# Kernel tuning notes

Measured on AMD Instinct MI355X. Metric: run time of the kernel, lower is better.

Reference implementation:

```python
import jax, jax.numpy as jnp
import numpy as np

B, N, DIM, H, DH = 8, 1024, 1024, 16, 64

def setup_inputs() -> dict:
    key = jax.random.key(0)
    ks = jax.random.split(key, 6)
    return {
        'x': jax.random.normal(ks[0], (B, N, DIM), dtype=jnp.float32),
        'freqs': jax.random.normal(ks[1], (1, N, DH), dtype=jnp.float32),
        'bias': jax.random.normal(ks[2], (1, N, DH), dtype=jnp.float32),
        'ln_gamma': jnp.ones((DIM,), jnp.float32),
        'ln_beta': jnp.zeros((DIM,), jnp.float32),
        'w_qk': jax.random.normal(ks[3], (DIM, 2 * H * DH), dtype=jnp.float32) * (DIM ** -0.5),
        'w_v': jax.random.normal(ks[4], (DIM, H * DH), dtype=jnp.float32) * (DIM ** -0.5),
        'w_out': jax.random.normal(ks[5], (H * DH, DIM), dtype=jnp.float32) * ((H * DH) ** -0.5),
        'b_out': jnp.zeros((DIM,), jnp.float32),
    }

def _apply_polar(t, freqs):
    # t: [b,h,n,d]; freqs: [1,n,d] broadcast over b,h. Output doubles last dim.
    t = jax.nn.softplus(t)
    return jnp.concatenate((t * jnp.cos(freqs), t * jnp.sin(freqs)), axis=-1)

def reference(x, freqs, bias, ln_gamma, ln_beta, w_qk, w_v, w_out, b_out):
    eps = 1e-5
    mu = jnp.mean(x, axis=-1, keepdims=True)
    var = jnp.var(x, axis=-1, keepdims=True)
    xn = (x - mu) * jax.lax.rsqrt(var + eps) * ln_gamma + ln_beta
    qk = jnp.einsum('bnd,de->bne', xn, w_qk)
    q, k = jnp.split(qk, 2, axis=-1)
    v = jnp.einsum('bnd,de->bne', xn, w_v)
    split_heads = lambda t: t.reshape(B, N, H, DH).transpose(0, 2, 1, 3)
    q, k, v = split_heads(q), split_heads(k), split_heads(v)
    q = _apply_polar(q, freqs)          # [b,h,n,2*DH]
    k = _apply_polar(k, freqs + bias)   # [b,h,n,2*DH]
    scale = DH ** -0.5
    dots = jnp.einsum('bhnd,bhmd->bhnm', q, k) * scale
    attn = jax.nn.softmax(dots, axis=-1)
    out = jnp.einsum('bhnm,bhmd->bhnd', attn, v)
    out = out.transpose(0, 2, 1, 3).reshape(B, N, H * DH)
    return jnp.einsum('bne,ed->bnd', out, w_out) + b_out
```

## Files before the change

kernel.cpp:

```cpp
#include <hip/hip_runtime.h>
#include <cmath>

using f16   = _Float16;
using f16x2 = __attribute__((ext_vector_type(2))) _Float16;
using f16x4 = __attribute__((ext_vector_type(4))) _Float16;
using f16x8 = __attribute__((ext_vector_type(8))) _Float16;
using f32x4 = __attribute__((ext_vector_type(4))) float;

#define DEV __device__ __forceinline__

constexpr int Bb  = 8;
constexpr int Nn  = 1024;
constexpr int DIM = 1024;
constexpr int Hh  = 16;
constexpr int DH  = 64;
constexpr int EQKV = 3072;

DEV void async16(const f16* g, f16* l) {
  __builtin_amdgcn_global_load_lds(
      (const __attribute__((address_space(1))) void*)g,
      (__attribute__((address_space(3))) void*)l, 16, 0, 0);
}

DEV float softplusf(float x) {
  return fmaxf(x, 0.f) + __logf(1.f + __expf(-fabsf(x)));
}

__global__ __launch_bounds__(256) void transpose_cvt3(const float* __restrict__ s0,
                                                      const float* __restrict__ s1,
                                                      const float* __restrict__ s2,
                                                      f16* __restrict__ d0,
                                                      f16* __restrict__ d2) {
  __shared__ float tile[32][33];
  const float* src; f16* dst; int cols;
  int bz = blockIdx.z;
  if (bz == 0)      { src = s0; dst = d0;                        cols = 2048; }
  else if (bz == 1) { src = s1; dst = d0 + (size_t)2048 * 1024;  cols = 1024; }
  else              { src = s2; dst = d2;                        cols = 1024; }
  int c0 = blockIdx.x * 32, r0 = blockIdx.y * 32;
  if (c0 >= cols) return;
  int t = threadIdx.x, tx = t & 31, ty = t >> 5;
#pragma unroll
  for (int j = 0; j < 32; j += 8)
    tile[ty + j][tx] = src[(size_t)(r0 + ty + j) * cols + c0 + tx];
  __syncthreads();
#pragma unroll
  for (int j = 0; j < 32; j += 8)
    dst[(size_t)(c0 + ty + j) * 1024 + r0 + tx] = (f16)tile[tx][ty + j];
}

__global__ __launch_bounds__(256) void ln_kernel(const float* __restrict__ x,
                                                 const float* __restrict__ gamma,
                                                 const float* __restrict__ beta,
                                                 f16* __restrict__ xn) {
  int row = blockIdx.x;
  int t = threadIdx.x;
  const float4* xr = (const float4*)(x + (size_t)row * DIM);
  float4 v = xr[t];
  float s  = v.x + v.y + v.z + v.w;
  float s2 = v.x * v.x + v.y * v.y + v.z * v.z + v.w * v.w;
#pragma unroll
  for (int off = 32; off; off >>= 1) {
    s  += __shfl_xor(s,  off, 64);
    s2 += __shfl_xor(s2, off, 64);
  }
  __shared__ float red[8];
  int wv = t >> 6, lane = t & 63;
  if (lane == 0) { red[wv] = s; red[4 + wv] = s2; }
  __syncthreads();
  s  = red[0] + red[1] + red[2] + red[3];
  s2 = red[4] + red[5] + red[6] + red[7];
  float mu  = s * (1.f / DIM);
  float var = s2 * (1.f / DIM) - mu * mu;
  float rs  = rsqrtf(var + 1e-5f);
  float4 g = ((const float4*)gamma)[t];
  float4 bb = ((const float4*)beta)[t];
  f16x4 o;
  o[0] = (f16)((v.x - mu) * rs * g.x + bb.x);
  o[1] = (f16)((v.y - mu) * rs * g.y + bb.y);
  o[2] = (f16)((v.z - mu) * rs * g.z + bb.z);
  o[3] = (f16)((v.w - mu) * rs * g.w + bb.w);
  ((f16x4*)(xn + (size_t)row * DIM))[t] = o;
}

template <bool FP32OUT>
__global__ __launch_bounds__(256) void gemm_bt(const f16* __restrict__ A,
                                               const f16* __restrict__ Bt,
                                               void* __restrict__ Cv,
                                               const float* __restrict__ bias,
                                               int M, int K, int E) {
  __shared__ f16 lA[128 * 32];
  __shared__ f16 lB[128 * 32];
  int tid  = threadIdx.x;
  int lane = tid & 63;
  int wv   = __builtin_amdgcn_readfirstlane(tid >> 6);
  int nbe  = E >> 7;
  int bm = blockIdx.x / nbe, be = blockIdx.x % nbe;
  size_t m0 = (size_t)bm * 128, e0 = (size_t)be * 128;
  int wm = (wv & 1) * 64, we = (wv >> 1) * 64;
  int lm = lane & 15, q = lane >> 4;

  f32x4 acc[4][4] = {};

  int row_s[2], cg_s[2];
#pragma unroll
  for (int r = 0; r < 2; ++r) {
    int s = r * 256 + tid;
    row_s[r] = s >> 2;
    cg_s[r]  = (s & 3) ^ ((row_s[r] >> 1) & 3);
  }
  const f16* pa[4];
  const f16* pb[4];
#pragma unroll
  for (int i = 0; i < 4; ++i) {
    int ra = wm + i * 16 + lm;
    pa[i] = lA + ra * 32 + (q ^ ((ra >> 1) & 3)) * 8;
    int rb = we + i * 16 + lm;
    pb[i] = lB + rb * 32 + (q ^ ((rb >> 1) & 3)) * 8;
  }

  for (int k0 = 0; k0 < K; k0 += 32) {
#pragma unroll
    for (int r = 0; r < 2; ++r) {
      const f16* ga = A  + (m0 + row_s[r]) * K + k0 + cg_s[r] * 8;
      const f16* gb = Bt + (e0 + row_s[r]) * K + k0 + cg_s[r] * 8;
      async16(ga, lA + (r * 256 + wv * 64) * 8);
      async16(gb, lB + (r * 256 + wv * 64) * 8);
    }
    __syncthreads();
    f16x8 af[4], bf[4];
#pragma unroll
    for (int i = 0; i < 4; ++i) {
      af[i] = *(const f16x8*)pa[i];
      bf[i] = *(const f16x8*)pb[i];
    }
#pragma unroll
    for (int i = 0; i < 4; ++i)
#pragma unroll
      for (int j = 0; j < 4; ++j)
        acc[i][j] = __builtin_amdgcn_mfma_f32_16x16x32_f16(af[i], bf[j], acc[i][j], 0, 0, 0);
    __syncthreads();
  }

#pragma unroll
  for (int i = 0; i < 4; ++i) {
    size_t mbase = m0 + wm + i * 16 + q * 4;
#pragma unroll
    for (int j = 0; j < 4; ++j) {
      size_t e = e0 + we + j * 16 + lm;
#pragma unroll
      for (int g = 0; g < 4; ++g) {
        float val = acc[i][j][g];
        if (FP32OUT)
          ((float*)Cv)[(mbase + g) * (size_t)E + e] = val + bias[e];
        else
          ((f16*)Cv)[(mbase + g) * (size_t)E + e] = (f16)val;
      }
    }
  }
}

__global__ __launch_bounds__(256) void polar_kernel(const f16* __restrict__ qkv,
                                                    const float* __restrict__ freqs,
                                                    const float* __restrict__ fbias,
                                                    f16* __restrict__ Qp,
                                                    f16* __restrict__ Kp,
                                                    f16* __restrict__ Vt) {
  __shared__ f16 vt[64 * 66];
  int tid = threadIdx.x;
  int bx = blockIdx.x;
  int nt = bx & 15, bh = bx >> 4;
  int b = bh >> 4, h = bh & 15;
  size_t tok0 = (size_t)b * Nn + nt * 64;
  int n0 = nt * 64;
  constexpr float kScale = 0.125f;
#pragma unroll
  for (int i = 0; i < 8; ++i) {
    int e2 = tid + i * 256;
    int nl = e2 >> 5, dp = (e2 & 31) * 2;
    size_t src = (tok0 + nl) * EQKV + h * 64 + dp;
    f16x2 q2 = *(const f16x2*)(qkv + src);
    f16x2 k2 = *(const f16x2*)(qkv + src + 1024);
    f16x2 v2 = *(const f16x2*)(qkv + src + 2048);
    int fidx = (n0 + nl) * 64 + dp;
    float2 f2  = *(const float2*)(freqs + fidx);
    float2 fb2 = *(const float2*)(fbias + fidx);
    f16x2 qc, qs, kc, ksn;
#pragma unroll
    for (int u = 0; u < 2; ++u) {
      float fq = u ? f2.y : f2.x;
      float fk = fq + (u ? fb2.y : fb2.x);
      float spq = softplusf((float)q2[u]) * kScale;
      float spk = softplusf((float)k2[u]);
      float snq, csq, snk, csk;
      __sincosf(fq, &snq, &csq);
      __sincosf(fk, &snk, &csk);
      qc[u]  = (f16)(spq * csq);
      qs[u]  = (f16)(spq * snq);
      kc[u]  = (f16)(spk * csk);
      ksn[u] = (f16)(spk * snk);
    }
    size_t dst = ((size_t)bh * Nn + n0 + nl) * 128 + dp;
    *(f16x2*)(Qp + dst)      = qc;
    *(f16x2*)(Qp + dst + 64) = qs;
    *(f16x2*)(Kp + dst)      = kc;
    *(f16x2*)(Kp + dst + 64) = ksn;
    vt[dp * 66 + nl]       = v2[0];
    vt[(dp + 1) * 66 + nl] = v2[1];
  }
  __syncthreads();
#pragma unroll
  for (int i = 0; i < 16; ++i) {
    int e = tid + i * 256;
    int d = e >> 6, nl = e & 63;
    Vt[((size_t)bh * 64 + d) * Nn + n0 + nl] = vt[d * 66 + nl];
  }
}

constexpr int VK0 = 0;
constexpr int VK1 = 8192;
constexpr int VV0 = 16384;
constexpr int VV1 = 21504;
constexpr int VEND = 26624;

__global__ __launch_bounds__(256, 3) void attn_kernel(const f16* __restrict__ Qp,
                                                      const f16* __restrict__ Kp,
                                                      const f16* __restrict__ Vt,
                                                      f16* __restrict__ attout) {
  __shared__ f16 smem[VEND];

  int tid = threadIdx.x, lane = tid & 63;
  int wv = __builtin_amdgcn_readfirstlane(tid >> 6);
  int lm = lane & 15, q = lane >> 4;
  int bx = blockIdx.x;
  int bh = (bx & 7) | ((bx >> 6) << 3);
  int qt = (bx >> 3) & 7;
  const f16* Kbase = Kp + (size_t)bh * Nn * 128;
  const f16* Vbase = Vt + (size_t)bh * 64 * Nn;

  {
    int idx = tid * 4;
    f16 val = (idx < 64) ? (f16)1.0f : (f16)0.0f;
    f16x4 v4 = {val, val, val, val};
    *(f16x4*)(smem + VV0 + 64 * 64 + idx) = v4;
    *(f16x4*)(smem + VV1 + 64 * 64 + idx) = v4;
  }

#pragma unroll
  for (int i = 0; i < 4; ++i) {
    int s = i * 256 + tid;
    int r = s >> 4, c = s & 15;
    int g = c ^ (r & 15);
    async16(Kbase + (size_t)r * 128 + g * 8, smem + VK0 + (i * 256 + wv * 64) * 8);
  }
#pragma unroll
  for (int i = 0; i < 2; ++i) {
    int s = i * 256 + tid;
    int r = s >> 3, c = s & 7;
    int g = c ^ (r & 7);
    async16(Vbase + (size_t)r * Nn + g * 8, smem + VV0 + (i * 256 + wv * 64) * 8);
  }

  f16x8 qf[2][4];
  {
    const f16* Qb = Qp + ((size_t)bh * Nn + qt * 128 + wv * 32) * 128;
#pragma unroll
    for (int grp = 0; grp < 2; ++grp)
#pragma unroll
      for (int ks = 0; ks < 4; ++ks)
        qf[grp][ks] = *(const f16x8*)(Qb + (size_t)(grp * 16 + lm) * 128 + ks * 32 + q * 8);
  }

  f32x4 O[2][5] = {};
  float mrow[2] = {-INFINITY, -INFINITY};

  for (int kt = 0; kt < 16; ++kt) {
    __syncthreads();

    if (kt < 15) {
      f16* nK = smem + ((kt & 1) ? VK0 : VK1);
      f16* nV = smem + ((kt & 1) ? VV0 : VV1);
#pragma unroll
      for (int i = 0; i < 4; ++i) {
        int s = i * 256 + tid;
        int r = s >> 4, c = s & 15;
        int g = c ^ (r & 15);
        async16(Kbase + (size_t)((kt + 1) * 64 + r) * 128 + g * 8, nK + (i * 256 + wv * 64) * 8);
      }
#pragma unroll
      for (int i = 0; i < 2; ++i) {
        int s = i * 256 + tid;
        int r = s >> 3, c = s & 7;
        int g = c ^ (r & 7);
        async16(Vbase + (size_t)r * Nn + (kt + 1) * 64 + g * 8, nV + (i * 256 + wv * 64) * 8);
      }
    }
    const f16* sK = smem + ((kt & 1) ? VK1 : VK0);
    const f16* sV = smem + ((kt & 1) ? VV1 : VV0);

    f32x4 S[2][4] = {};
#pragma unroll
    for (int nt = 0; nt < 4; ++nt) {
      f16x8 kf[4];
#pragma unroll
      for (int ks = 0; ks < 4; ++ks)
        kf[ks] = *(const f16x8*)(sK + (nt * 16 + lm) * 128 + (((ks * 4 + q) ^ lm) * 8));
#pragma unroll
      for (int ks = 0; ks < 4; ++ks) {
        S[0][nt] = __builtin_amdgcn_mfma_f32_16x16x32_f16(kf[ks], qf[0][ks], S[0][nt], 0, 0, 0);
        S[1][nt] = __builtin_amdgcn_mfma_f32_16x16x32_f16(kf[ks], qf[1][ks], S[1][nt], 0, 0, 0);
      }
    }

    f16x4 pf[2][4];
#pragma unroll
    for (int grp = 0; grp < 2; ++grp) {
      float mx = -INFINITY;
#pragma unroll
      for (int nt = 0; nt < 4; ++nt)
#pragma unroll
        for (int g = 0; g < 4; ++g) mx = fmaxf(mx, S[grp][nt][g]);
      mx = fmaxf(mx, __shfl_xor(mx, 16, 64));
      mx = fmaxf(mx, __shfl_xor(mx, 32, 64));
      float mn = fmaxf(mrow[grp], mx);
      float alpha = __expf(mrow[grp] - mn);
      mrow[grp] = mn;
#pragma unroll
      for (int nt = 0; nt < 4; ++nt)
#pragma unroll
        for (int g = 0; g < 4; ++g)
          pf[grp][nt][g] = (f16)__expf(S[grp][nt][g] - mn);
#pragma unroll
      for (int nto = 0; nto < 5; ++nto)
#pragma unroll
        for (int g = 0; g < 4; ++g) O[grp][nto][g] *= alpha;
    }

#pragma unroll
    for (int nto = 0; nto < 5; ++nto) {
      int r = nto * 16 + lm;
#pragma unroll
      for (int nt = 0; nt < 4; ++nt) {
        int c16 = (nt * 2 + (q >> 1)) ^ (r & 7);
        f16x4 vf = *(const f16x4*)(sV + r * 64 + c16 * 8 + (q & 1) * 4);
        O[0][nto] = __builtin_amdgcn_mfma_f32_16x16x16f16(vf, pf[0][nt], O[0][nto], 0, 0, 0);
        O[1][nto] = __builtin_amdgcn_mfma_f32_16x16x16f16(vf, pf[1][nt], O[1][nto], 0, 0, 0);
      }
    }
  }

  int b = bh >> 4, h = bh & 15;
#pragma unroll
  for (int grp = 0; grp < 2; ++grp) {
    float l = __shfl(O[grp][4][0], lm, 64);
    float inv = 1.f / l;
    size_t token = (size_t)b * Nn + qt * 128 + wv * 32 + grp * 16 + lm;
#pragma unroll
    for (int nto = 0; nto < 4; ++nto) {
      f16x4 o4;
#pragma unroll
      for (int g = 0; g < 4; ++g) o4[g] = (f16)(O[grp][nto][g] * inv);
      *(f16x4*)(attout + token * (size_t)(Hh * DH) + h * 64 + nto * 16 + q * 4) = o4;
    }
  }
}

extern "C" void kernel_launch(void* const* d_in, const int* in_sizes, int n_in,
                              void* d_out, int out_size, void* d_ws, size_t ws_size,
                              hipStream_t stream) {
  const float* x     = (const float*)d_in[0];
  const float* freqs = (const float*)d_in[1];
  const float* fbias = (const float*)d_in[2];
  const float* gamma = (const float*)d_in[3];
  const float* beta  = (const float*)d_in[4];
  const float* w_qk  = (const float*)d_in[5];
  const float* w_v   = (const float*)d_in[6];
  const float* w_out = (const float*)d_in[7];
  const float* b_out = (const float*)d_in[8];
  float* out = (float*)d_out;

  const size_t T = (size_t)Bb * Nn;
  f16* WqkvT = (f16*)d_ws;
  f16* WoutT = WqkvT + (size_t)EQKV * DIM;
  f16* Xn    = WoutT + (size_t)DIM * DIM;
  f16* QKV   = Xn + T * DIM;
  f16* AttO  = QKV + T * EQKV;
  f16* Qp    = AttO + T * DIM;
  f16* Kp    = Qp + (size_t)128 * Nn * 128;
  f16* Vt    = Kp + (size_t)128 * Nn * 128;

  transpose_cvt3<<<dim3(64, 32, 3), 256, 0, stream>>>(w_qk, w_v, w_out, WqkvT, WoutT);

  ln_kernel<<<(int)T, 256, 0, stream>>>(x, gamma, beta, Xn);

  gemm_bt<false><<<(int)(T / 128) * (EQKV / 128), 256, 0, stream>>>(
      Xn, WqkvT, (void*)QKV, nullptr, (int)T, DIM, EQKV);

  polar_kernel<<<Bb * Hh * (Nn / 64), 256, 0, stream>>>(QKV, freqs, fbias, Qp, Kp, Vt);

  attn_kernel<<<Bb * Hh * (Nn / 128), 256, 0, stream>>>(Qp, Kp, Vt, AttO);

  gemm_bt<true><<<(int)(T / 128) * (DIM / 128), 256, 0, stream>>>(
      AttO, WoutT, (void*)out, b_out, (int)T, DIM, DIM);
}
```

Baseline: 312.8 us.

## Use 256x256-tile double-buffered GEMM with staged async loads for QKV projection

Adds a new 512-thread GEMM kernel with 256x256 output tiles, an XOR-swizzled LDS layout, double buffering, and global_load_lds prefetches split into stages that interleave with MFMA groups. A block-id swizzle groups tiles for L2 locality. It replaces the 128x128 GEMM for the QKV projection only, aiming for higher arithmetic intensity and better overlap of loads with compute. The cost is 128KB of LDS per block and a larger accumulator register footprint, which may limit occupancy.

Result: faster. 301.5 us (-3.6%).

```diff
diff --git a/kernel.cpp b/kernel.cpp
--- a/kernel.cpp
+++ b/kernel.cpp
@@ -160,6 +160,150 @@
   }
 }
 
+template <bool FP32OUT>
+__global__ __launch_bounds__(512, 2) void gemm256(const f16* __restrict__ A,
+                                                  const f16* __restrict__ Bt,
+                                                  void* __restrict__ Cv,
+                                                  const float* __restrict__ bias,
+                                                  int M, int K, int E) {
+  __shared__ f16 sm[65536];
+  const int tid  = threadIdx.x;
+  const int lane = tid & 63;
+  const int wv   = __builtin_amdgcn_readfirstlane(tid >> 6);
+  const int lm   = lane & 15, q = lane >> 4;
+  const int wrow = (wv >> 2) * 128;
+  const int wcol = (wv & 3) * 64;
+
+  const int nbe = E >> 8;
+  const int cpx = gridDim.x >> 3;
+  const int bid = blockIdx.x;
+  const int swz = (bid & 7) * cpx + (bid >> 3);
+  const int bm = swz / nbe, be = swz % nbe;
+  const size_t m0 = (size_t)bm * 256, e0 = (size_t)be * 256;
+
+  const int rl  = lane >> 3;
+  const int pcp = lane & 7;
+  const int cg  = pcp ^ rl;
+  const f16* aS = A  + (m0 + (size_t)(wv * 8 + rl)) * K + cg * 8;
+  const f16* bS = Bt + (e0 + (size_t)((wv >> 2) * 64 + (wv & 3) * 8 + rl)) * K + cg * 8;
+  const int aDofs = wv * 512;
+  const int bDofs = 16384 + ((wv >> 2) * 64 + (wv & 3) * 8) * 64;
+
+  const int x0 = ((0 + q) ^ (lm & 7)) * 8;
+  const int x1 = ((4 + q) ^ (lm & 7)) * 8;
+
+  const int NT = K >> 6;
+
+  async16(aS,                     sm + aDofs);
+  async16(aS + (size_t)128 * K,   sm + aDofs + 128 * 64);
+  async16(bS,                     sm + bDofs);
+  async16(bS + (size_t)128 * K,   sm + bDofs + 128 * 64);
+  async16(bS + (size_t)32 * K,    sm + bDofs + 32 * 64);
+  async16(bS + (size_t)160 * K,   sm + bDofs + 160 * 64);
+  async16(aS + (size_t)64 * K,    sm + aDofs + 64 * 64);
+  async16(aS + (size_t)192 * K,   sm + aDofs + 192 * 64);
+
+  f32x4 acc[8][4] = {};
+  f16x8 af[4][2], bf[4][2];
+
+  for (int t = 0; t < NT; ++t) {
+    const int b = t & 1, nb = b ^ 1;
+    const int tn = (t + 1 < NT) ? t + 1 : t;
+    const f16* pA = sm + b * 32768;
+    const f16* pB = pA + 16384;
+    f16* aD = sm + nb * 32768 + aDofs;
+    f16* bD = sm + nb * 32768 + bDofs;
+    const f16* aSk = aS + tn * 64;
+    const f16* bSk = bS + tn * 64;
+
+    async16(aSk,                   aD);
+    async16(aSk + (size_t)128 * K, aD + 128 * 64);
+    asm volatile("s_waitcnt vmcnt(6)" ::: "memory");
+    __builtin_amdgcn_s_barrier();
+#pragma unroll
+    for (int i = 0; i < 4; ++i) {
+      const f16* p = pA + (wrow + i * 16 + lm) * 64;
+      af[i][0] = *(const f16x8*)(p + x0);
+      af[i][1] = *(const f16x8*)(p + x1);
+    }
+#pragma unroll
+    for (int j = 0; j < 2; ++j) {
+      const f16* p = pB + (wcol + j * 16 + lm) * 64;
+      bf[j][0] = *(const f16x8*)(p + x0);
+      bf[j][1] = *(const f16x8*)(p + x1);
+    }
+    __builtin_amdgcn_s_setprio(1);
+#pragma unroll
+    for (int i = 0; i < 4; ++i)
+#pragma unroll
+      for (int j = 0; j < 2; ++j) {
+        acc[i][j] = __builtin_amdgcn_mfma_f32_16x16x32_f16(af[i][0], bf[j][0], acc[i][j], 0, 0, 0);
+        acc[i][j] = __builtin_amdgcn_mfma_f32_16x16x32_f16(af[i][1], bf[j][1], acc[i][j], 0, 0, 0);
+      }
+    __builtin_amdgcn_s_setprio(0);
+
+    async16(bSk,                   bD);
+    async16(bSk + (size_t)128 * K, bD + 128 * 64);
+    asm volatile("s_waitcnt vmcnt(6)" ::: "memory");
+    __builtin_amdgcn_s_barrier();
+#pragma unroll
+    for (int j = 0; j < 2; ++j) {
+      const f16* p = pB + (wcol + 32 + j * 16 + lm) * 64;
+      bf[2 + j][0] = *(const f16x8*)(p + x0);
+      bf[2 + j][1] = *(const f16x8*)(p + x1);
+    }
+    __builtin_amdgcn_s_setprio(1);
+#pragma unroll
+    for (int i = 0; i < 4; ++i)
+#pragma unroll
+      for (int j = 2; j < 4; ++j) {
+        acc[i][j] = __builtin_amdgcn_mfma_f32_16x16x32_f16(af[i][0], bf[j][0], acc[i][j], 0, 0, 0);
+        acc[i][j] = __builtin_amdgcn_mfma_f32_16x16x32_f16(af[i][1], bf[j][1], acc[i][j], 0, 0, 0);
+      }
+    __builtin_amdgcn_s_setprio(0);
+
+    async16(bSk + (size_t)32 * K,  bD + 32 * 64);
+    async16(bSk + (size_t)160 * K, bD + 160 * 64);
+    async16(aSk + (size_t)64 * K,  aD + 64 * 64);
+    async16(aSk + (size_t)192 * K, aD + 192 * 64);
+    asm volatile("s_waitcnt vmcnt(8)" ::: "memory");
+    __builtin_amdgcn_s_barrier();
+#pragma unroll
+    for (int i = 0; i < 4; ++i) {
+      const f16* p = pA + (wrow + 64 + i * 16 + lm) * 64;
+      af[i][0] = *(const f16x8*)(p + x0);
+      af[i][1] = *(const f16x8*)(p + x1);
+    }
+    __builtin_amdgcn_s_setprio(1);
+#pragma unroll
+    for (int i = 0; i < 4; ++i)
+#pragma unroll
+      for (int j = 0; j < 4; ++j) {
+        acc[4 + i][j] = __builtin_amdgcn_mfma_f32_16x16x32_f16(af[i][0], bf[j][0], acc[4 + i][j], 0, 0, 0);
+        acc[4 + i][j] = __builtin_amdgcn_mfma_f32_16x16x32_f16(af[i][1], bf[j][1], acc[4 + i][j], 0, 0, 0);
+      }
+    __builtin_amdgcn_s_setprio(0);
+  }
+  asm volatile("s_waitcnt vmcnt(0)" ::: "memory");
+
+#pragma unroll
+  for (int ii = 0; ii < 8; ++ii) {
+    size_t mrow = m0 + wrow + (ii >> 2) * 64 + (ii & 3) * 16 + q * 4;
+#pragma unroll
+    for (int j = 0; j < 4; ++j) {
+      size_t e = e0 + wcol + j * 16 + lm;
+#pragma unroll
+      for (int g = 0; g < 4; ++g) {
+        float val = acc[ii][j][g];
+        if (FP32OUT)
+          ((float*)Cv)[(mrow + g) * (size_t)E + e] = val + bias[e];
+        else
+          ((f16*)Cv)[(mrow + g) * (size_t)E + e] = (f16)val;
+      }
+    }
+  }
+}
+
 __global__ __launch_bounds__(256) void polar_kernel(const f16* __restrict__ qkv,
                                                     const float* __restrict__ freqs,
                                                     const float* __restrict__ fbias,
@@ -393,7 +537,7 @@
 
   ln_kernel<<<(int)T, 256, 0, stream>>>(x, gamma, beta, Xn);
 
-  gemm_bt<false><<<(int)(T / 128) * (EQKV / 128), 256, 0, stream>>>(
+  gemm256<false><<<(int)(T / 256) * (EQKV / 256), 512, 0, stream>>>(
       Xn, WqkvT, (void*)QKV, nullptr, (int)T, DIM, EQKV);
 
   polar_kernel<<<Bb * Hh * (Nn / 64), 256, 0, stream>>>(QKV, freqs, fbias, Qp, Kp, Vt);
```

## Fuse softplus-polar epilogue into a wider-tile QKV GEMM with a precomputed trig table

Applied to the files above, without the earlier changes.

Replaces the generic QKV GEMM plus the separate polar kernel with a dedicated 128x256-tile GEMM. Its epilogue applies softplus, the q scale and cos/sin directly, writing Qp/Kp in an interleaved (cos,sin) layout. V is written in plain token-major form and transposed by a slimmed kernel. A small prep kernel precomputes cos/sin of freqs and freqs+bias once into a float4 table. The goal is to avoid writing and re-reading the full fp16 QKV intermediate and to recompute no trig per batch/head. The cost is a heavier epilogue with scattered 4-byte stores, extra registers from the larger tile, and one extra tiny launch.

Result: slower. 394.5 us (+26.1%).

```diff
diff --git a/kernel.cpp b/kernel.cpp
--- a/kernel.cpp
+++ b/kernel.cpp
@@ -47,6 +47,17 @@
 #pragma unroll
   for (int j = 0; j < 32; j += 8)
     dst[(size_t)(c0 + ty + j) * 1024 + r0 + tx] = (f16)tile[tx][ty + j];
+}
+
+__global__ __launch_bounds__(256) void trig_prep(const float* __restrict__ freqs,
+                                                 const float* __restrict__ fbias,
+                                                 float4* __restrict__ trig) {
+  int i = blockIdx.x * 256 + threadIdx.x;
+  float f = freqs[i], fb = fbias[i];
+  float cq, sq, ck, sk;
+  __sincosf(f, &sq, &cq);
+  __sincosf(f + fb, &sk, &ck);
+  trig[i] = make_float4(cq, sq, ck, sk);
 }
 
 __global__ __launch_bounds__(256) void ln_kernel(const float* __restrict__ x,
@@ -160,12 +171,121 @@
   }
 }
 
-__global__ __launch_bounds__(256) void polar_kernel(const f16* __restrict__ qkv,
-                                                    const float* __restrict__ freqs,
-                                                    const float* __restrict__ fbias,
-                                                    f16* __restrict__ Qp,
-                                                    f16* __restrict__ Kp,
-                                                    f16* __restrict__ Vt) {
+__global__ __launch_bounds__(256, 3) void gemm_qkv(const f16* __restrict__ A,
+                                                   const f16* __restrict__ Bt,
+                                                   f16* __restrict__ Qp,
+                                                   f16* __restrict__ Kp,
+                                                   f16* __restrict__ Vn,
+                                                   const float4* __restrict__ trig,
+                                                   int M, int K) {
+  __shared__ f16 sm[24576];
+  const int tid  = threadIdx.x;
+  const int lane = tid & 63;
+  const int wv   = __builtin_amdgcn_readfirstlane(tid >> 6);
+  const int lm   = lane & 15, q = lane >> 4;
+  const int wrow = (wv >> 1) * 64;
+  const int wcol = (wv & 1) * 128;
+
+  const int nbe = EQKV >> 8;
+  const int cpx = gridDim.x >> 3;
+  const int bid = blockIdx.x;
+  const int swz = (bid & 7) * cpx + (bid >> 3);
+  const int bm = swz / nbe, be = swz % nbe;
+  const size_t m0 = (size_t)bm * 128, e0 = (size_t)be * 256;
+
+  const int rl = tid >> 2, pc = tid & 3;
+  const int cg = pc ^ ((rl >> 1) & 3);
+  const f16* aS = A  + (m0 + rl) * K + cg * 8;
+  const f16* bS = Bt + (e0 + rl) * K + cg * 8;
+  const int aDo = tid * 8;
+  const int bDo = 4096 + tid * 8;
+
+  const int x = (q ^ ((lm >> 1) & 3)) * 8;
+
+  const int NT = K >> 5;
+
+  async16(aS,                  sm + aDo);
+  async16(aS + (size_t)64 * K, sm + aDo + 2048);
+  async16(bS,                  sm + bDo);
+  async16(bS + (size_t)64 * K, sm + bDo + 2048);
+  async16(bS + (size_t)128 * K, sm + bDo + 4096);
+  async16(bS + (size_t)192 * K, sm + bDo + 6144);
+
+  f32x4 acc[4][8] = {};
+
+  for (int t = 0; t < NT; ++t) {
+    const int b = t & 1;
+    __syncthreads();
+
+    if (t + 1 < NT) {
+      f16* nB = sm + (b ^ 1) * 12288;
+      const int k = (t + 1) * 32;
+      async16(aS + k,                  nB + aDo);
+      async16(aS + (size_t)64 * K + k, nB + aDo + 2048);
+      async16(bS + k,                  nB + bDo);
+      async16(bS + (size_t)64 * K + k, nB + bDo + 2048);
+      async16(bS + (size_t)128 * K + k, nB + bDo + 4096);
+      async16(bS + (size_t)192 * K + k, nB + bDo + 6144);
+    }
+
+    const f16* pA = sm + b * 12288;
+    const f16* pB = pA + 4096;
+    f16x8 bf[8], af[4];
+#pragma unroll
+    for (int j = 0; j < 8; ++j)
+      bf[j] = *(const f16x8*)(pB + (wcol + j * 16 + lm) * 32 + x);
+#pragma unroll
+    for (int i = 0; i < 4; ++i)
+      af[i] = *(const f16x8*)(pA + (wrow + i * 16 + lm) * 32 + x);
+#pragma unroll
+    for (int i = 0; i < 4; ++i)
+#pragma unroll
+      for (int j = 0; j < 8; ++j)
+        acc[i][j] = __builtin_amdgcn_mfma_f32_16x16x32_f16(af[i], bf[j], acc[i][j], 0, 0, 0);
+  }
+
+  const int sec = be >> 2;
+  if (sec < 2) {
+    f16* dst = (sec == 0) ? Qp : Kp;
+    const float scl = (sec == 0) ? 0.125f : 1.0f;
+#pragma unroll
+    for (int i = 0; i < 4; ++i) {
+      size_t mrow = m0 + wrow + i * 16 + q * 4;
+#pragma unroll
+      for (int j = 0; j < 8; ++j) {
+        int hd = (int)((e0 + wcol + j * 16 + lm) & 1023);
+        int h = hd >> 6, d = hd & 63;
+#pragma unroll
+        for (int g = 0; g < 4; ++g) {
+          size_t tok = mrow + g;
+          int n = (int)(tok & 1023);
+          size_t bh = (tok >> 10) * 16 + h;
+          float sp = softplusf(acc[i][j][g]) * scl;
+          float4 T = trig[n * 64 + d];
+          float c = (sec == 0) ? T.x : T.z;
+          float s = (sec == 0) ? T.y : T.w;
+          f16x2 o = { (f16)(sp * c), (f16)(sp * s) };
+          *(f16x2*)(dst + (bh * (size_t)Nn + n) * 128 + 2 * d) = o;
+        }
+      }
+    }
+  } else {
+#pragma unroll
+    for (int i = 0; i < 4; ++i) {
+      size_t mrow = m0 + wrow + i * 16 + q * 4;
+#pragma unroll
+      for (int j = 0; j < 8; ++j) {
+        int hd = (int)((e0 + wcol + j * 16 + lm) & 1023);
+#pragma unroll
+        for (int g = 0; g < 4; ++g)
+          Vn[(mrow + g) * 1024 + hd] = (f16)acc[i][j][g];
+      }
+    }
+  }
+}
+
+__global__ __launch_bounds__(256) void vtrans_kernel(const f16* __restrict__ Vn,
+                                                     f16* __restrict__ Vt) {
   __shared__ f16 vt[64 * 66];
   int tid = threadIdx.x;
   int bx = blockIdx.x;
@@ -173,38 +293,11 @@
   int b = bh >> 4, h = bh & 15;
   size_t tok0 = (size_t)b * Nn + nt * 64;
   int n0 = nt * 64;
-  constexpr float kScale = 0.125f;
 #pragma unroll
   for (int i = 0; i < 8; ++i) {
     int e2 = tid + i * 256;
     int nl = e2 >> 5, dp = (e2 & 31) * 2;
-    size_t src = (tok0 + nl) * EQKV + h * 64 + dp;
-    f16x2 q2 = *(const f16x2*)(qkv + src);
-    f16x2 k2 = *(const f16x2*)(qkv + src + 1024);
-    f16x2 v2 = *(const f16x2*)(qkv + src + 2048);
-    int fidx = (n0 + nl) * 64 + dp;
-    float2 f2  = *(const float2*)(freqs + fidx);
-    float2 fb2 = *(const float2*)(fbias + fidx);
-    f16x2 qc, qs, kc, ksn;
-#pragma unroll
-    for (int u = 0; u < 2; ++u) {
-      float fq = u ? f2.y : f2.x;
-      float fk = fq + (u ? fb2.y : fb2.x);
-      float spq = softplusf((float)q2[u]) * kScale;
-      float spk = softplusf((float)k2[u]);
-      float snq, csq, snk, csk;
-      __sincosf(fq, &snq, &csq);
-      __sincosf(fk, &snk, &csk);
-      qc[u]  = (f16)(spq * csq);
-      qs[u]  = (f16)(spq * snq);
-      kc[u]  = (f16)(spk * csk);
-      ksn[u] = (f16)(spk * snk);
-    }
-    size_t dst = ((size_t)bh * Nn + n0 + nl) * 128 + dp;
-    *(f16x2*)(Qp + dst)      = qc;
-    *(f16x2*)(Qp + dst + 64) = qs;
-    *(f16x2*)(Kp + dst)      = kc;
-    *(f16x2*)(Kp + dst + 64) = ksn;
+    f16x2 v2 = *(const f16x2*)(Vn + (tok0 + nl) * 1024 + h * 64 + dp);
     vt[dp * 66 + nl]       = v2[0];
     vt[(dp + 1) * 66 + nl] = v2[1];
   }
@@ -382,21 +475,24 @@
   const size_t T = (size_t)Bb * Nn;
   f16* WqkvT = (f16*)d_ws;
   f16* WoutT = WqkvT + (size_t)EQKV * DIM;
-  f16* Xn    = WoutT + (size_t)DIM * DIM;
-  f16* QKV   = Xn + T * DIM;
-  f16* AttO  = QKV + T * EQKV;
+  float4* trig = (float4*)(WoutT + (size_t)DIM * DIM);
+  f16* Xn    = (f16*)(trig + (size_t)Nn * DH);
+  f16* Vn    = Xn + T * DIM;
+  f16* AttO  = Vn + T * DIM;
   f16* Qp    = AttO + T * DIM;
   f16* Kp    = Qp + (size_t)128 * Nn * 128;
   f16* Vt    = Kp + (size_t)128 * Nn * 128;
 
   transpose_cvt3<<<dim3(64, 32, 3), 256, 0, stream>>>(w_qk, w_v, w_out, WqkvT, WoutT);
 
+  trig_prep<<<(Nn * DH) / 256, 256, 0, stream>>>(freqs, fbias, trig);
+
   ln_kernel<<<(int)T, 256, 0, stream>>>(x, gamma, beta, Xn);
 
-  gemm_bt<false><<<(int)(T / 128) * (EQKV / 128), 256, 0, stream>>>(
-      Xn, WqkvT, (void*)QKV, nullptr, (int)T, DIM, EQKV);
-
-  polar_kernel<<<Bb * Hh * (Nn / 64), 256, 0, stream>>>(QKV, freqs, fbias, Qp, Kp, Vt);
+  gemm_qkv<<<(int)(T / 128) * (EQKV / 256), 256, 0, stream>>>(
+      Xn, WqkvT, Qp, Kp, Vn, trig, (int)T, DIM);
+
+  vtrans_kernel<<<Bb * Hh * (Nn / 64), 256, 0, stream>>>(Vn, Vt);
 
   attn_kernel<<<Bb * Hh * (Nn / 128), 256, 0, stream>>>(Qp, Kp, Vt, AttO);
 
```
